# Performance work log

Measured on AMD Instinct MI355X. Metric: run time of the kernel, lower is better.

## Reference

```python
import jax, jax.numpy as jnp
import numpy as np

B, N, D, H, DH, F, L, LC = 32, 256, 512, 8, 64, 2048, 8, 2
NEG = -1e9
SCALE = 1.0 / float(np.sqrt(DH))


def _ln(x, g, b, eps=1e-3):
    # keras LayerNormalization default epsilon=1e-3
    m = jnp.mean(x, -1, keepdims=True)
    v = jnp.mean((x - m) ** 2, -1, keepdims=True)
    return (x - m) * jax.lax.rsqrt(v + eps) * g + b


def setup_inputs() -> dict:
    key = jax.random.key(0)
    ks = jax.random.split(key, 20)
    n = lambda k, s: jax.random.normal(k, s, dtype=jnp.float32) * 0.02
    lengths = jax.random.randint(ks[0], (B,), N // 2, N + 1)
    mask = jnp.arange(N)[None, :] < lengths[:, None]  # [B,N] bool
    return {
        'x': jax.random.normal(ks[1], (B, N, D), dtype=jnp.float32),
        'interaction': jax.random.normal(ks[2], (B, N, N, H), dtype=jnp.float32) * 0.1,
        'class_token': n(ks[3], (1, 1, D)),
        'p_ln1_g': jnp.ones((L, D)), 'p_ln1_b': jnp.zeros((L, D)),
        'p_wq': n(ks[4], (L, D, D)), 'p_wk': n(ks[5], (L, D, D)),
        'p_wv': n(ks[6], (L, D, D)), 'p_wo': n(ks[7], (L, D, D)),
        'p_ln2_g': jnp.ones((L, D)), 'p_ln2_b': jnp.zeros((L, D)),
        'p_w1': n(ks[8], (L, D, F)), 'p_b1': jnp.zeros((L, F)),
        'p_w2': n(ks[9], (L, F, D)), 'p_b2': jnp.zeros((L, D)),
        'c_ln1_g': jnp.ones((LC, D)), 'c_ln1_b': jnp.zeros((LC, D)),
        'c_qk': n(ks[10], (LC, D, H, DH)), 'c_qb': jnp.zeros((LC, H, DH)),
        'c_kk': n(ks[11], (LC, D, H, DH)), 'c_kb': jnp.zeros((LC, H, DH)),
        'c_vk': n(ks[12], (LC, D, H, DH)), 'c_vb': jnp.zeros((LC, H, DH)),
        'c_ok': n(ks[13], (LC, H, DH, D)), 'c_ob': jnp.zeros((LC, D)),
        'c_ln2_g': jnp.ones((LC, D)), 'c_ln2_b': jnp.zeros((LC, D)),
        'c_w1': n(ks[14], (LC, D, F)), 'c_b1': jnp.zeros((LC, F)),
        'c_w2': n(ks[15], (LC, F, D)), 'c_b2': jnp.zeros((LC, D)),
        'mask': mask,
    }


def _part_forward(x, interaction, class_token, p_ln1_g, p_ln1_b, p_wq, p_wk, p_wv, p_wo,
                  p_ln2_g, p_ln2_b, p_w1, p_b1, p_w2, p_b2,
                  c_ln1_g, c_ln1_b, c_qk, c_qb, c_kk, c_kb, c_vk, c_vb, c_ok, c_ob,
                  c_ln2_g, c_ln2_b, c_w1, c_b1, c_w2, c_b2, mask):
    # pairwise particle mask [B,1,N,N]; keras Softmax adds (1-mask)*-1e9
    pmask = (mask[:, None, None, :] & mask[:, None, :, None]).astype(x.dtype)
    padd = (1.0 - pmask) * NEG
    inter = jnp.transpose(interaction, (0, 3, 1, 2))  # [B,H,N,N]
    h = x
    for i in range(L):
        # pre-LN interaction self-attention (dropout inactive at inference)
        hn = _ln(h, p_ln1_g[i], p_ln1_b[i])
        q = (hn @ p_wq[i]).reshape(B, N, H, DH)
        k = (hn @ p_wk[i]).reshape(B, N, H, DH)
        v = (hn @ p_wv[i]).reshape(B, N, H, DH)
        s = jnp.einsum('bqhd,bkhd->bhqk', q, k) * SCALE + inter + padd
        a = jax.nn.softmax(s, axis=-1)
        o = jnp.einsum('bhqk,bkhd->bqhd', a, v).reshape(B, N, D) @ p_wo[i]
        h = h + o
        # pre-LN FFN, gelu (exact, tf.nn.gelu default)
        fn = _ln(h, p_ln2_g[i], p_ln2_b[i])
        h = h + (jax.nn.gelu(fn @ p_w1[i] + p_b1[i], approximate=False) @ p_w2[i] + p_b2[i])
    query = jnp.broadcast_to(class_token, (B, 1, D)).astype(x.dtype)
    cmask = jnp.concatenate([jnp.ones((B, 1), bool), mask], axis=1)[:, None, None, :].astype(x.dtype)
    cadd = (1.0 - cmask) * NEG  # [B,1,1,N+1]
    for i in range(LC):
        # class-attention: K/V from LN(concat([token, particles])), Q from RAW token (as in source)
        cat = jnp.concatenate([query, h], axis=1)  # [B,N+1,D]
        cn = _ln(cat, c_ln1_g[i], c_ln1_b[i])
        qh = jnp.einsum('bqd,dhk->bqhk', query, c_qk[i]) + c_qb[i]
        kh = jnp.einsum('bsd,dhk->bshk', cn, c_kk[i]) + c_kb[i]
        vh = jnp.einsum('bsd,dhk->bshk', cn, c_vk[i]) + c_vb[i]
        s = jnp.einsum('bqhk,bshk->bhqs', qh, kh) * SCALE + cadd
        a = jax.nn.softmax(s, axis=-1)
        o = jnp.einsum('bhqs,bshk->bqhk', a, vh)
        o = jnp.einsum('bqhk,hkd->bqd', o, c_ok[i]) + c_ob[i]
        query = query + o
        fn = _ln(query, c_ln2_g[i], c_ln2_b[i])
        query = query + (jax.nn.gelu(fn @ c_w1[i] + c_b1[i], approximate=False) @ c_w2[i] + c_b2[i])
    return query  # [B,1,D]


def reference(x, interaction, class_token, p_ln1_g, p_ln1_b, p_wq, p_wk, p_wv, p_wo,
              p_ln2_g, p_ln2_b, p_w1, p_b1, p_w2, p_b2,
              c_ln1_g, c_ln1_b, c_qk, c_qb, c_kk, c_kb, c_vk, c_vb, c_ok, c_ob,
              c_ln2_g, c_ln2_b, c_w1, c_b1, c_w2, c_b2, mask):
    return _part_forward(x, interaction, class_token, p_ln1_g, p_ln1_b, p_wq, p_wk, p_wv, p_wo,
                         p_ln2_g, p_ln2_b, p_w1, p_b1, p_w2, p_b2,
                         c_ln1_g, c_ln1_b, c_qk, c_qb, c_kk, c_kb, c_vk, c_vb, c_ok, c_ob,
                         c_ln2_g, c_ln2_b, c_w1, c_b1, c_w2, c_b2, mask)
```

## Files before the change

kernel.cpp:

```cpp
#include <hip/hip_runtime.h>
#include <hip/hip_fp16.h>

#define B_ 32
#define N_ 256
#define D_ 512
#define H_ 8
#define DH_ 64
#define F_ 2048
#define L_ 8
#define LC_ 2
#define NEG_ (-1e9f)
#define SCALE_ 0.125f
#define LDSK 72
#define KCH_ 128

typedef unsigned short u16;
typedef unsigned int u32;
typedef long long s64;
typedef __attribute__((ext_vector_type(8))) short bf16x8;
typedef __attribute__((ext_vector_type(8))) unsigned short u16x8;
typedef __attribute__((ext_vector_type(4))) float f32x4;

__device__ __forceinline__ float b2f(u16 u) {
    union { u32 i; float f; } v; v.i = ((u32)u) << 16; return v.f;
}
__device__ __forceinline__ u16 f2b(float f) {
    union { float f; u32 i; } v; v.f = f;
    u32 x = v.i;
    u32 r = (x + 0x7FFFu + ((x >> 16) & 1u)) >> 16;
    return (u16)r;
}
__device__ __forceinline__ float h2f(u16 u) {
    __half_raw hr; hr.x = u;
    return __half2float(__half(hr));
}
__device__ __forceinline__ void gld16(u16* lds, const u16* g) {
    __builtin_amdgcn_global_load_lds(
        (const __attribute__((address_space(1))) u16*)g,
        (__attribute__((address_space(3))) u16*)lds, 16, 0, 0);
}
__device__ __forceinline__ float ldf(const void* p, size_t i, int fl) {
    if (fl == 1) return ((const float*)p)[i];
    if (fl == 0) return b2f(((const u16*)p)[i]);
    return h2f(((const u16*)p)[i]);
}
__device__ __forceinline__ void ld4(const void* p, size_t i, int fl, float o[4]) {
    if (fl == 1) {
        const float4 v = *(const float4*)((const float*)p + i);
        o[0] = v.x; o[1] = v.y; o[2] = v.z; o[3] = v.w;
    } else if (fl == 0) {
        const ushort4 v = *(const ushort4*)((const u16*)p + i);
        o[0] = b2f(v.x); o[1] = b2f(v.y); o[2] = b2f(v.z); o[3] = b2f(v.w);
    } else {
        const ushort4 v = *(const ushort4*)((const u16*)p + i);
        o[0] = h2f(v.x); o[1] = h2f(v.y); o[2] = h2f(v.z); o[3] = h2f(v.w);
    }
}

__global__ void sniff_kernel(const u32* __restrict__ g1, int* __restrict__ flag) {
    if (threadIdx.x == 0 && blockIdx.x == 0) {
        u32 w = g1[0];
        int f = 0;
        if (w == 0x3F800000u) f = 1;
        else if (w == 0x3C003C00u) f = 2;
        flag[0] = f;
    }
}

__global__ void mask_decode_kernel(const unsigned char* __restrict__ raw,
                                   float* __restrict__ mf) {
    int i = blockIdx.x * 256 + threadIdx.x;
    if (i >= B_ * N_) return;
    unsigned char c0 = raw[0], c1 = raw[1], c4 = raw[4];
    bool v;
    if (c1 == 0x3F || c1 == 0x3C) {
        v = ((const u16*)raw)[i] != 0;
    } else if (c0 == 1 && c1 == 1) {
        v = raw[i] != 0;
    } else if (c0 == 1 && c1 == 0) {
        if (c4 == 1) v = ((const int*)raw)[i] != 0;
        else v = ((const long long*)raw)[i] != 0;
    } else {
        v = ((const float*)raw)[i] != 0.0f;
    }
    mf[i] = v ? 1.0f : 0.0f;
}

__global__ void cvt_in_kernel(const void* __restrict__ in, float* __restrict__ out,
                              int n, const int* __restrict__ fl) {
    int i = blockIdx.x * 256 + threadIdx.x;
    if (i < n) out[i] = ldf(in, (size_t)i, fl[0]);
}
__global__ void bcast_token_kernel(const void* __restrict__ ct, float* __restrict__ qry,
                                   const int* __restrict__ fl) {
    int i = blockIdx.x * 256 + threadIdx.x;
    qry[i] = ldf(ct, (size_t)(i & (D_ - 1)), fl[0]);
}
__global__ void out_copy_kernel(const float* __restrict__ in, float* __restrict__ out, int n) {
    int i = blockIdx.x * 256 + threadIdx.x;
    if (i < n) out[i] = in[i];
}
__global__ void concat_bias_kernel(const void* __restrict__ b1, s64 o1,
                                   const void* __restrict__ b2, s64 o2,
                                   float* __restrict__ dst, const int* __restrict__ flp) {
    int i = blockIdx.x * 256 + threadIdx.x;
    if (i < 512) dst[i] = ldf(b1, (size_t)(o1 + i), flp[0]);
    else if (i < 1024) dst[i] = ldf(b2, (size_t)(o2 + i - 512), flp[0]);
}

__global__ __launch_bounds__(256) void inter_t_kernel(const void* __restrict__ inter,
                                                      const float* __restrict__ mf,
                                                      u16* __restrict__ out,
                                                      const int* __restrict__ flp) {
    __shared__ float tile[256][9];
    __shared__ float mks[256];
    int fl = flp[0];
    int bq = blockIdx.x;
    int b = bq >> 8, q = bq & 255;
    int t = threadIdx.x;
    size_t base = (size_t)bq * 2048;
#pragma unroll
    for (int p = 0; p < 8; ++p) {
        int e = p * 256 + t;
        tile[e >> 3][e & 7] = ldf(inter, base + e, fl);
    }
    mks[t] = mf[b * 256 + t];
    __syncthreads();
    float mq = mf[b * 256 + q];
    int h = t >> 5;
    int k0 = (t & 31) * 8;
    u16x8 v8;
#pragma unroll
    for (int ii = 0; ii < 8; ++ii) {
        int k = k0 + ii;
        float v = tile[k][h];
        if (mq * mks[k] < 0.5f) v += NEG_;
        v8[ii] = (short)f2b(v);
    }
    *(u16x8*)(out + (((size_t)(b * 8 + h) * 256 + q) * 256 + k0)) = v8;
}

__global__ __launch_bounds__(256) void transpose_w_kernel(const void* __restrict__ W, s64 weoff,
                                                          int Nst, int Kd,
                                                          u16* __restrict__ wt,
                                                          const int* __restrict__ flp) {
    __shared__ float tile[32][33];
    int fl = flp[0];
    int n0 = blockIdx.x * 32, k0 = blockIdx.y * 32;
    int tr = threadIdx.x >> 5, tc = threadIdx.x & 31;
#pragma unroll
    for (int p = 0; p < 4; ++p) {
        int kk = p * 8 + tr;
        tile[kk][tc] = ldf(W, (size_t)(weoff + (s64)(k0 + kk) * Nst + n0 + tc), fl);
    }
    __syncthreads();
#pragma unroll
    for (int p = 0; p < 4; ++p) {
        int nn = p * 8 + tr;
        wt[(s64)(n0 + nn) * Kd + k0 + tc] = f2b(tile[tc][nn]);
    }
}

__global__ __launch_bounds__(256) void twt6_kernel(const void* __restrict__ wq,
                                                   const void* __restrict__ wk,
                                                   const void* __restrict__ wv,
                                                   const void* __restrict__ wo,
                                                   const void* __restrict__ w1,
                                                   const void* __restrict__ w2,
                                                   s64 off44, s64 offw1, s64 offw2,
                                                   u16* __restrict__ wtqkv,
                                                   u16* __restrict__ wto,
                                                   u16* __restrict__ wt1,
                                                   u16* __restrict__ wt2,
                                                   const int* __restrict__ flp) {
    __shared__ float tile[32][33];
    int fl = flp[0];
    int bid = blockIdx.x;
    const void* W; s64 weoff; int Nst, Kd; u16* dst; int lb;
    if (bid < 256)       { W = wq; weoff = off44; Nst = 512;  Kd = 512;  dst = wtqkv;          lb = bid; }
    else if (bid < 512)  { W = wk; weoff = off44; Nst = 512;  Kd = 512;  dst = wtqkv + 262144; lb = bid - 256; }
    else if (bid < 768)  { W = wv; weoff = off44; Nst = 512;  Kd = 512;  dst = wtqkv + 524288; lb = bid - 512; }
    else if (bid < 1024) { W = wo; weoff = off44; Nst = 512;  Kd = 512;  dst = wto;            lb = bid - 768; }
    else if (bid < 2048) { W = w1; weoff = offw1; Nst = 2048; Kd = 512;  dst = wt1;            lb = bid - 1024; }
    else                 { W = w2; weoff = offw2; Nst = 512;  Kd = 2048; dst = wt2;            lb = bid - 2048; }
    int nx = Nst >> 5;
    int n0 = (lb % nx) << 5, k0 = (lb / nx) << 5;
    int tr = threadIdx.x >> 5, tc = threadIdx.x & 31;
#pragma unroll
    for (int p = 0; p < 4; ++p) {
        int kk = p * 8 + tr;
        tile[kk][tc] = ldf(W, (size_t)(weoff + (s64)(k0 + kk) * Nst + n0 + tc), fl);
    }
    __syncthreads();
#pragma unroll
    for (int p = 0; p < 4; ++p) {
        int nn = p * 8 + tr;
        dst[(s64)(n0 + nn) * Kd + k0 + tc] = f2b(tile[tc][nn]);
    }
}

__global__ __launch_bounds__(256) void ln_kernel(const float* __restrict__ in,
                                                 const void* __restrict__ g,
                                                 const void* __restrict__ bta,
                                                 s64 peoff,
                                                 u16* __restrict__ out,
                                                 const int* __restrict__ flp) {
    __shared__ float ws4[4];
    __shared__ float wsq[4];
    int fl = flp[0];
    size_t row = blockIdx.x;
    int t = threadIdx.x;
    float x0 = in[row * D_ + t];
    float x1 = in[row * D_ + 256 + t];
    float s = x0 + x1;
#pragma unroll
    for (int off = 32; off > 0; off >>= 1) s += __shfl_xor(s, off);
    if ((t & 63) == 0) ws4[t >> 6] = s;
    __syncthreads();
    float mean = (ws4[0] + ws4[1] + ws4[2] + ws4[3]) * (1.0f / D_);
    float d0 = x0 - mean, d1 = x1 - mean;
    float sq = d0 * d0 + d1 * d1;
#pragma unroll
    for (int off = 32; off > 0; off >>= 1) sq += __shfl_xor(sq, off);
    if ((t & 63) == 0) wsq[t >> 6] = sq;
    __syncthreads();
    float var = (wsq[0] + wsq[1] + wsq[2] + wsq[3]) * (1.0f / D_);
    float inv = 1.0f / sqrtf(var + 1e-3f);
    out[row * D_ + t]       = f2b(d0 * inv * ldf(g, peoff + t, fl)       + ldf(bta, peoff + t, fl));
    out[row * D_ + 256 + t] = f2b(d1 * inv * ldf(g, peoff + 256 + t, fl) + ldf(bta, peoff + 256 + t, fl));
}

__global__ __launch_bounds__(256) void ln_cat_kernel(const float* __restrict__ qry,
                                                     const float* __restrict__ h,
                                                     const void* __restrict__ g,
                                                     const void* __restrict__ bta,
                                                     s64 peoff,
                                                     u16* __restrict__ out,
                                                     const int* __restrict__ flp) {
    __shared__ float ws4[4];
    __shared__ float wsq[4];
    int fl = flp[0];
    size_t row = blockIdx.x;
    int b = (int)(row / 257);
    int r = (int)(row % 257);
    const float* src = (r == 0) ? (qry + (size_t)b * D_)
                                : (h + ((size_t)b * N_ + (r - 1)) * D_);
    int t = threadIdx.x;
    float x0 = src[t];
    float x1 = src[256 + t];
    float s = x0 + x1;
#pragma unroll
    for (int off = 32; off > 0; off >>= 1) s += __shfl_xor(s, off);
    if ((t & 63) == 0) ws4[t >> 6] = s;
    __syncthreads();
    float mean = (ws4[0] + ws4[1] + ws4[2] + ws4[3]) * (1.0f / D_);
    float d0 = x0 - mean, d1 = x1 - mean;
    float sq = d0 * d0 + d1 * d1;
#pragma unroll
    for (int off = 32; off > 0; off >>= 1) sq += __shfl_xor(sq, off);
    if ((t & 63) == 0) wsq[t >> 6] = sq;
    __syncthreads();
    float var = (wsq[0] + wsq[1] + wsq[2] + wsq[3]) * (1.0f / D_);
    float inv = 1.0f / sqrtf(var + 1e-3f);
    out[row * D_ + t]       = f2b(d0 * inv * ldf(g, peoff + t, fl)       + ldf(bta, peoff + t, fl));
    out[row * D_ + 256 + t] = f2b(d1 * inv * ldf(g, peoff + 256 + t, fl) + ldf(bta, peoff + 256 + t, fl));
}

__global__ __launch_bounds__(512) void mfma_gemm_t(const u16* __restrict__ A,
                                                   const u16* __restrict__ Wt,
                                                   int wst, int wkoff,
                                                   const void* __restrict__ bias, s64 beoff,
                                                   int bflag,
                                                   const float* __restrict__ res,
                                                   void* __restrict__ C, int cbf,
                                                   int M, int N, int K, int act,
                                                   const int* __restrict__ flp) {
    __shared__ u16 Alds[2 * 128 * 64];
    __shared__ u16 Blds[2 * 128 * 64];
    int tid = threadIdx.x;
    int gx = gridDim.x;
    int nwg = gx * gridDim.y;
    int orig = blockIdx.y * gx + blockIdx.x;
    int xcd = orig & 7;
    int qq = nwg >> 3, rr = nwg & 7;
    int wg = (xcd < rr ? xcd * (qq + 1) : rr * (qq + 1) + (xcd - rr) * qq) + (orig >> 3);
    int bx = wg % gx, by = wg / gx;
    int bm = by << 7, bn = bx << 7;
    int wid = tid >> 6, lane = tid & 63;
    int wm = (wid >> 2) << 6, wn = (wid & 3) << 5;
    int l15 = lane & 15, q = lane >> 4;
    f32x4 acc[4][2];
#pragma unroll
    for (int a = 0; a < 4; ++a)
#pragma unroll
        for (int b = 0; b < 2; ++b) acc[a][b] = (f32x4){0.f, 0.f, 0.f, 0.f};
    int srow = tid >> 3;
    int sseg = tid & 7;
    int xseg = sseg ^ (srow & 7);
    const u16* arow[2];
#pragma unroll
    for (int p = 0; p < 2; ++p) {
        int gr = bm + p * 64 + srow;
        if (gr >= M) gr = M - 1;
        arow[p] = A + (size_t)gr * K + (xseg << 3);
    }
    const u16* brow[2];
#pragma unroll
    for (int p = 0; p < 2; ++p)
        brow[p] = Wt + (size_t)(bn + p * 64 + srow) * wst + wkoff + (xseg << 3);
    int dstoff = srow * 64 + (sseg << 3);
    auto stage = [&](int buf, int k0) {
        u16* Ab = Alds + buf * 8192;
        u16* Bb = Blds + buf * 8192;
#pragma unroll
        for (int p = 0; p < 2; ++p) gld16(&Ab[dstoff + p * 4096], arow[p] + k0);
#pragma unroll
        for (int p = 0; p < 2; ++p) gld16(&Bb[dstoff + p * 4096], brow[p] + k0);
    };
    int nt = K >> 6;
    stage(0, 0);
    if (nt > 1) stage(1, 64);
    for (int t = 0; t < nt; ++t) {
        if (t + 1 < nt) asm volatile("s_waitcnt vmcnt(4)" ::: "memory");
        else            asm volatile("s_waitcnt vmcnt(0)" ::: "memory");
        __builtin_amdgcn_s_barrier();
        asm volatile("" ::: "memory");
        const u16* Ac = Alds + (t & 1) * 8192;
        const u16* Bc = Blds + (t & 1) * 8192;
#pragma unroll
        for (int ks = 0; ks < 2; ++ks) {
            int seg = ((ks * 4 + q) ^ (l15 & 7)) << 3;
            bf16x8 af[4], bfr[2];
#pragma unroll
            for (int mt = 0; mt < 4; ++mt)
                af[mt] = *(const bf16x8*)(&Ac[(wm + mt * 16 + l15) * 64 + seg]);
#pragma unroll
            for (int nt2 = 0; nt2 < 2; ++nt2)
                bfr[nt2] = *(const bf16x8*)(&Bc[(wn + nt2 * 16 + l15) * 64 + seg]);
#pragma unroll
            for (int mt = 0; mt < 4; ++mt)
#pragma unroll
                for (int nt2 = 0; nt2 < 2; ++nt2)
                    acc[mt][nt2] = __builtin_amdgcn_mfma_f32_16x16x32_bf16(
                        af[mt], bfr[nt2], acc[mt][nt2], 0, 0, 0);
        }
        asm volatile("" ::: "memory");
        __builtin_amdgcn_s_barrier();
        if (t + 2 < nt) stage(t & 1, (t + 2) << 6);
    }
    int fl = (bflag >= 0) ? bflag : flp[0];
#pragma unroll
    for (int nt2 = 0; nt2 < 2; ++nt2) {
        int col = bn + wn + nt2 * 16 + l15;
        float bv = bias ? ldf(bias, (size_t)(beoff + col), fl) : 0.f;
#pragma unroll
        for (int mt = 0; mt < 4; ++mt) {
#pragma unroll
            for (int i = 0; i < 4; ++i) {
                int row = bm + wm + mt * 16 + q * 4 + i;
                if (row >= M) continue;
                float c = acc[mt][nt2][i] + bv;
                if (act) c = 0.5f * c * (1.0f + erff(c * 0.70710678118654752f));
                if (res) c += res[(size_t)row * N + col];
                if (cbf) ((u16*)C)[(size_t)row * N + col] = f2b(c);
                else     ((float*)C)[(size_t)row * N + col] = c;
            }
        }
    }
}

__global__ __launch_bounds__(256) void skinny_gemm_kernel(const void* __restrict__ A, int abf,
                                                          const void* __restrict__ W, s64 weoff,
                                                          int wst,
                                                          float* __restrict__ Cp,
                                                          int N, int K,
                                                          const int* __restrict__ flp) {
    __shared__ float As[32 * KCH_];
    int wfl = flp[0];
    int tid = threadIdx.x;
    int bn = blockIdx.x << 6;
    int ks = blockIdx.y;
    int k0 = ks * KCH_;
#pragma unroll
    for (int p = 0; p < (32 * KCH_) / 1024; ++p) {
        int idx = p * 1024 + tid * 4;
        int m = idx >> 7, c = idx & (KCH_ - 1);
        size_t gi = (size_t)m * K + k0 + c;
        if (abf) {
            const ushort4 v = *(const ushort4*)((const u16*)A + gi);
            As[idx]     = b2f(v.x);
            As[idx + 1] = b2f(v.y);
            As[idx + 2] = b2f(v.z);
            As[idx + 3] = b2f(v.w);
        } else {
            *(float4*)&As[idx] = *(const float4*)((const float*)A + gi);
        }
    }
    __syncthreads();
    int tx = tid & 63, ty = tid >> 6;
    int n = bn + tx;
    float acc[8] = {0.f, 0.f, 0.f, 0.f, 0.f, 0.f, 0.f, 0.f};
#pragma unroll 4
    for (int kk = 0; kk < KCH_; kk += 4) {
        float w0 = ldf(W, (size_t)(weoff + (s64)(k0 + kk) * wst + n), wfl);
        float w1 = ldf(W, (size_t)(weoff + (s64)(k0 + kk + 1) * wst + n), wfl);
        float w2 = ldf(W, (size_t)(weoff + (s64)(k0 + kk + 2) * wst + n), wfl);
        float w3 = ldf(W, (size_t)(weoff + (s64)(k0 + kk + 3) * wst + n), wfl);
#pragma unroll
        for (int r = 0; r < 8; ++r) {
            const float4 a = *(const float4*)&As[(ty * 8 + r) * KCH_ + kk];
            acc[r] += a.x * w0 + a.y * w1 + a.z * w2 + a.w * w3;
        }
    }
#pragma unroll
    for (int r = 0; r < 8; ++r)
        Cp[((size_t)ks * 32 + ty * 8 + r) * N + n] = acc[r];
}

__global__ __launch_bounds__(256) void skinny_epi_kernel(const float* __restrict__ Cp,
                                                         int KS, int N,
                                                         const void* __restrict__ bias, s64 beoff,
                                                         const float* __restrict__ res,
                                                         float* __restrict__ C, int act,
                                                         const int* __restrict__ flp) {
    int i = blockIdx.x * 256 + threadIdx.x;
    if (i >= 32 * N) return;
    int n = i % N;
    float s = 0.f;
    for (int ks = 0; ks < KS; ++ks) s += Cp[(size_t)ks * 32 * N + i];
    if (bias) s += ldf(bias, (size_t)(beoff + n), flp[0]);
    if (act) s = 0.5f * s * (1.0f + erff(s * 0.70710678118654752f));
    if (res) s += res[i];
    C[i] = s;
}

__global__ __launch_bounds__(256) void attn_mfma_kernel(const u16* __restrict__ QKV,
                                                        const u16* __restrict__ IT,
                                                        u16* __restrict__ O) {
    __shared__ u16 KV[256 * 72];
    __shared__ u16 Amat[64 * 264];
    int li = blockIdx.y * 4 + blockIdx.x;
    int slot = li >> 3;
    int bh = (li & 7) * 32 + (slot >> 2);
    int q0 = (slot & 3) << 6;
    int b = bh >> 3, hh = bh & 7;
    int tid = threadIdx.x;
    int w = tid >> 6, l = tid & 63, q2 = l >> 4, l15 = l & 15;
    int qrow = q0 + (w << 4) + l15;
    const u16* qptr = QKV + (size_t)(b * N_ + qrow) * 1536 + hh * DH_ + (q2 << 3);
    bf16x8 aq0 = *(const bf16x8*)(qptr);
    bf16x8 aq1 = *(const bf16x8*)(qptr + 32);
    {
        int r = tid >> 3, seg = (tid & 7) << 3;
#pragma unroll
        for (int p = 0; p < 8; ++p) {
            int k = p * 32 + r;
            *(u16x8*)(&KV[k * LDSK + seg]) =
                *(const u16x8*)(QKV + (size_t)(b * N_ + k) * 1536 + 512 + hh * DH_ + seg);
        }
    }
    u16x8 vreg[8];
    {
        const u16* vptr = QKV + (size_t)(b * N_ + (w << 6)) * 1536 + 1024 + hh * DH_ + l;
#pragma unroll
        for (int s = 0; s < 8; ++s)
#pragma unroll
            for (int e = 0; e < 8; ++e)
                vreg[s][e] = vptr[(size_t)(s * 8 + e) * 1536];
    }
    const u16* itp = IT + ((size_t)bh * N_ + q0 + (w << 4) + (q2 << 2)) * N_ + l15;
    u16 itv0[16], itv1[16], itv2[16], itv3[16];
#pragma unroll
    for (int t = 0; t < 16; ++t) {
        itv0[t] = itp[t * 16];
        itv1[t] = itp[(size_t)N_ + t * 16];
        itv2[t] = itp[(size_t)2 * N_ + t * 16];
        itv3[t] = itp[(size_t)3 * N_ + t * 16];
    }
    asm volatile("s_waitcnt lgkmcnt(0)" ::: "memory");
    __builtin_amdgcn_s_barrier();
    __builtin_amdgcn_sched_barrier(0);
    f32x4 acc[16];
#pragma unroll
    for (int t = 0; t < 16; ++t) {
        const u16* kp = &KV[(t * 16 + l15) * LDSK + (q2 << 3)];
        bf16x8 b0 = *(const bf16x8*)(kp);
        bf16x8 b1 = *(const bf16x8*)(kp + 32);
        f32x4 z = (f32x4){0.f, 0.f, 0.f, 0.f};
        z = __builtin_amdgcn_mfma_f32_16x16x32_bf16(aq0, b0, z, 0, 0, 0);
        acc[t] = __builtin_amdgcn_mfma_f32_16x16x32_bf16(aq1, b1, z, 0, 0, 0);
    }
    asm volatile("s_waitcnt lgkmcnt(0)" ::: "memory");
    __builtin_amdgcn_s_barrier();
    __builtin_amdgcn_sched_barrier(0);
#pragma unroll
    for (int s = 0; s < 8; ++s)
        *(u16x8*)(&KV[l * 264 + (w << 6) + s * 8]) = vreg[s];
    float mx[4] = {-3e38f, -3e38f, -3e38f, -3e38f};
#pragma unroll
    for (int t = 0; t < 16; ++t) {
        float s0 = acc[t][0] * SCALE_ + b2f(itv0[t]);
        float s1 = acc[t][1] * SCALE_ + b2f(itv1[t]);
        float s2 = acc[t][2] * SCALE_ + b2f(itv2[t]);
        float s3 = acc[t][3] * SCALE_ + b2f(itv3[t]);
        acc[t][0] = s0; acc[t][1] = s1; acc[t][2] = s2; acc[t][3] = s3;
        mx[0] = fmaxf(mx[0], s0);
        mx[1] = fmaxf(mx[1], s1);
        mx[2] = fmaxf(mx[2], s2);
        mx[3] = fmaxf(mx[3], s3);
    }
#pragma unroll
    for (int i = 0; i < 4; ++i) {
        mx[i] = fmaxf(mx[i], __shfl_xor(mx[i], 1));
        mx[i] = fmaxf(mx[i], __shfl_xor(mx[i], 2));
        mx[i] = fmaxf(mx[i], __shfl_xor(mx[i], 4));
        mx[i] = fmaxf(mx[i], __shfl_xor(mx[i], 8));
    }
    float sum[4] = {0.f, 0.f, 0.f, 0.f};
#pragma unroll
    for (int t = 0; t < 16; ++t)
#pragma unroll
        for (int i = 0; i < 4; ++i) {
            float e = expf(acc[t][i] - mx[i]);
            acc[t][i] = e;
            sum[i] += e;
        }
#pragma unroll
    for (int i = 0; i < 4; ++i) {
        sum[i] += __shfl_xor(sum[i], 1);
        sum[i] += __shfl_xor(sum[i], 2);
        sum[i] += __shfl_xor(sum[i], 4);
        sum[i] += __shfl_xor(sum[i], 8);
        sum[i] = 1.0f / sum[i];
    }
#pragma unroll
    for (int t = 0; t < 16; ++t)
#pragma unroll
        for (int i = 0; i < 4; ++i)
            Amat[((w << 4) + (q2 << 2) + i) * 264 + t * 16 + l15] = f2b(acc[t][i] * sum[i]);
    asm volatile("s_waitcnt lgkmcnt(0)" ::: "memory");
    __builtin_amdgcn_s_barrier();
    __builtin_amdgcn_sched_barrier(0);
    f32x4 pacc[4];
#pragma unroll
    for (int dt = 0; dt < 4; ++dt) pacc[dt] = (f32x4){0.f, 0.f, 0.f, 0.f};
#pragma unroll
    for (int kc = 0; kc < 8; ++kc) {
        bf16x8 af = *(const bf16x8*)(&Amat[((w << 4) + l15) * 264 + kc * 32 + (q2 << 3)]);
#pragma unroll
        for (int dt = 0; dt < 4; ++dt) {
            bf16x8 bf = *(const bf16x8*)(&KV[(dt * 16 + l15) * 264 + kc * 32 + (q2 << 3)]);
            pacc[dt] = __builtin_amdgcn_mfma_f32_16x16x32_bf16(af, bf, pacc[dt], 0, 0, 0);
        }
    }
    u16* ob = O + (size_t)(b * N_ + q0 + (w << 4) + (q2 << 2)) * D_ + hh * DH_ + l15;
#pragma unroll
    for (int dt = 0; dt < 4; ++dt)
#pragma unroll
        for (int i = 0; i < 4; ++i)
            ob[(size_t)i * D_ + dt * 16] = f2b(pacc[dt][i]);
}

__global__ __launch_bounds__(256) void cls_attn_kernel(const float* __restrict__ qh,
                                                       const u16* __restrict__ kvh,
                                                       const float* __restrict__ mf,
                                                       float* __restrict__ O) {
    __shared__ float qs[64];
    __shared__ float am[257];
    __shared__ float wred[4];
    __shared__ float vred[256];
    int b = blockIdx.x >> 3, hh = blockIdx.x & 7;
    int t = threadIdx.x;
    int w = t >> 6, l = t & 63;
    if (t < 64) qs[t] = qh[(size_t)b * D_ + hh * DH_ + t];
    __syncthreads();
    const u16* krow = kvh + (size_t)(b * 257 + t) * 1024 + hh * DH_;
    float s = 0.f;
#pragma unroll
    for (int seg = 0; seg < 8; ++seg) {
        u16x8 kv8 = *(const u16x8*)(krow + seg * 8);
#pragma unroll
        for (int e = 0; e < 8; ++e) s += qs[seg * 8 + e] * b2f(kv8[e]);
    }
    float cm = (t == 0) ? 1.0f : mf[b * N_ + t - 1];
    s = s * SCALE_ + ((cm > 0.5f) ? 0.0f : NEG_);
    float s256 = -1e30f;
    if (t == 0) {
        const u16* krow2 = kvh + (size_t)(b * 257 + 256) * 1024 + hh * DH_;
        float s2 = 0.f;
#pragma unroll
        for (int seg = 0; seg < 8; ++seg) {
            u16x8 kv8 = *(const u16x8*)(krow2 + seg * 8);
#pragma unroll
            for (int e = 0; e < 8; ++e) s2 += qs[seg * 8 + e] * b2f(kv8[e]);
        }
        float cm2 = mf[b * N_ + 255];
        s256 = s2 * SCALE_ + ((cm2 > 0.5f) ? 0.0f : NEG_);
    }
    float mx = (t == 0) ? fmaxf(s, s256) : s;
#pragma unroll
    for (int off = 32; off > 0; off >>= 1) mx = fmaxf(mx, __shfl_xor(mx, off));
    if (l == 0) wred[w] = mx;
    __syncthreads();
    mx = fmaxf(fmaxf(wred[0], wred[1]), fmaxf(wred[2], wred[3]));
    float p = expf(s - mx);
    float p256 = (t == 0) ? expf(s256 - mx) : 0.f;
    float sum = p + p256;
#pragma unroll
    for (int off = 32; off > 0; off >>= 1) sum += __shfl_xor(sum, off);
    __syncthreads();
    if (l == 0) wred[w] = sum;
    __syncthreads();
    float invs = 1.0f / (wred[0] + wred[1] + wred[2] + wred[3]);
    am[t] = p * invs;
    if (t == 0) am[256] = p256 * invs;
    __syncthreads();
    int g = w, d = l;
    const u16* vcol = kvh + (size_t)(b * 257 + g * 64) * 1024 + 512 + hh * DH_ + d;
    float acc = 0.f;
#pragma unroll 8
    for (int j = 0; j < 64; ++j)
        acc += am[g * 64 + j] * b2f(vcol[(size_t)j * 1024]);
    if (g == 3)
        acc += am[256] * b2f(kvh[(size_t)(b * 257 + 256) * 1024 + 512 + hh * DH_ + d]);
    vred[t] = acc;
    __syncthreads();
    if (t < 64)
        O[(size_t)b * D_ + hh * DH_ + t] = vred[t] + vred[64 + t] + vred[128 + t] + vred[192 + t];
}

extern "C" void kernel_launch(void* const* d_in, const int* in_sizes, int n_in,
                              void* d_out, int out_size, void* d_ws, size_t ws_size,
                              hipStream_t stream) {
    const void* x           = d_in[0];
    const void* interaction = d_in[1];
    const void* class_token = d_in[2];
    const void* p_ln1_g = d_in[3];
    const void* p_ln1_b = d_in[4];
    const void* p_wq    = d_in[5];
    const void* p_wk    = d_in[6];
    const void* p_wv    = d_in[7];
    const void* p_wo    = d_in[8];
    const void* p_ln2_g = d_in[9];
    const void* p_ln2_b = d_in[10];
    const void* p_w1    = d_in[11];
    const void* p_b1    = d_in[12];
    const void* p_w2    = d_in[13];
    const void* p_b2    = d_in[14];
    const void* c_ln1_g = d_in[15];
    const void* c_ln1_b = d_in[16];
    const void* c_qk    = d_in[17];
    const void* c_qb    = d_in[18];
    const void* c_kk    = d_in[19];
    const void* c_kb    = d_in[20];
    const void* c_vk    = d_in[21];
    const void* c_vb    = d_in[22];
    const void* c_ok    = d_in[23];
    const void* c_ob    = d_in[24];
    const void* c_ln2_g = d_in[25];
    const void* c_ln2_b = d_in[26];
    const void* c_w1    = d_in[27];
    const void* c_b1    = d_in[28];
    const void* c_w2    = d_in[29];
    const void* c_b2    = d_in[30];
    const unsigned char* maskraw = (const unsigned char*)d_in[31];

    const size_t NT  = (size_t)B_ * N_;
    const size_t NTD = NT * D_;

    char* base = (char*)d_ws;
    int*   flag   = (int*)base;
    float* maskf  = (float*)(base + 64);
    float* h      = (float*)(base + 64 + 32768);
    u16*   hn     = (u16*)(h + NTD);
    u16*   qkv    = hn + (size_t)B_ * 257 * D_;
    float* qry    = (float*)(qkv + (size_t)8192 * 1536);
    float* qh     = qry + 16384;
    float* ocls   = qh + 16384;
    u16*   fnq    = (u16*)(ocls + 16384);
    float* midc   = (float*)(fnq + 16384);
    float* biaskv = midc + 65536;
    u16*   wt     = (u16*)(biaskv + 1024);
    u16*   wtqkv = wt;
    u16*   wto   = wt + 786432;
    u16*   wt1   = wt + 1048576;
    u16*   wt2   = wt + 2097152;
    u16*   inter_t = wt + 3145728;
    u16*   midp  = qkv;
    float* cpart = (float*)(qkv + (size_t)8224 * 1024);

    auto mgemm = [&](const u16* A, const u16* Wt, int wst, int wkoff,
                     const void* bias, s64 beoff, int bflag, const float* res, void* C, int cbf,
                     int M, int N, int K, int act) {
        dim3 grid(N / 128, (M + 127) / 128);
        mfma_gemm_t<<<grid, 512, 0, stream>>>(A, Wt, wst, wkoff, bias, beoff, bflag,
                                              res, C, cbf, M, N, K, act, flag);
    };
    auto skgemm = [&](const void* A, int abf, const void* W, s64 weoff, int wst,
                      const void* bias, s64 beoff, const float* res, float* C,
                      int N, int K, int act) {
        int KS = K / KCH_;
        skinny_gemm_kernel<<<dim3(N / 64, KS), 256, 0, stream>>>(A, abf, W, weoff, wst,
                                                                 cpart, N, K, flag);
        skinny_epi_kernel<<<(32 * N + 255) / 256, 256, 0, stream>>>(cpart, KS, N, bias, beoff,
                                                                    res, C, act, flag);
    };
    auto twt = [&](const void* W, s64 weoff, int Nst, int Kd, u16* dst) {
        dim3 grid(Nst / 32, Kd / 32);
        transpose_w_kernel<<<grid, 256, 0, stream>>>(W, weoff, Nst, Kd, dst, flag);
    };

    sniff_kernel<<<1, 64, 0, stream>>>((const u32*)p_ln1_g, flag);
    mask_decode_kernel<<<32, 256, 0, stream>>>(maskraw, maskf);
    inter_t_kernel<<<8192, 256, 0, stream>>>(interaction, maskf, inter_t, flag);
    cvt_in_kernel<<<(int)(NTD / 256), 256, 0, stream>>>(x, h, (int)NTD, flag);
    bcast_token_kernel<<<64, 256, 0, stream>>>(class_token, qry, flag);

    for (int i = 0; i < L_; ++i) {
        s64 wo = (s64)i * D_ * D_;
        twt6_kernel<<<3072, 256, 0, stream>>>(p_wq, p_wk, p_wv, p_wo, p_w1, p_w2,
                                              wo, (s64)i * D_ * F_, (s64)i * F_ * D_,
                                              wtqkv, wto, wt1, wt2, flag);
        ln_kernel<<<(int)NT, 256, 0, stream>>>(h, p_ln1_g, p_ln1_b, (s64)i * D_, hn, flag);
        mgemm(hn, wtqkv, D_, 0, nullptr, 0, -1, nullptr, qkv, 1, (int)NT, 1536, D_, 0);
        attn_mfma_kernel<<<dim3(4, B_ * H_), 256, 0, stream>>>(qkv, inter_t, hn);
        mgemm(hn, wto, D_, 0, nullptr, 0, -1, h, h, 0, (int)NT, D_, D_, 0);
        ln_kernel<<<(int)NT, 256, 0, stream>>>(h, p_ln2_g, p_ln2_b, (s64)i * D_, hn, flag);
        for (int c = 0; c < 2; ++c) {
            mgemm(hn, wt1 + (s64)c * 1024 * 512, D_, 0,
                  p_b1, (s64)i * F_ + c * 1024, -1, nullptr, midp, 1,
                  (int)NT, 1024, D_, 1);
            mgemm(midp, wt2, F_, c * 1024,
                  (c == 0) ? p_b2 : nullptr, (s64)i * D_, -1, h, h, 0,
                  (int)NT, D_, 1024, 0);
        }
    }

    for (int i = 0; i < LC_; ++i) {
        s64 wo = (s64)i * D_ * D_;
        twt(c_kk, wo, D_, D_, wtqkv);
        twt(c_vk, wo, D_, D_, wtqkv + 262144);
        concat_bias_kernel<<<4, 256, 0, stream>>>(c_kb, (s64)i * D_, c_vb, (s64)i * D_, biaskv, flag);
        ln_cat_kernel<<<B_ * 257, 256, 0, stream>>>(qry, h, c_ln1_g, c_ln1_b, (s64)i * D_, hn, flag);
        skgemm(qry, 0, c_qk, wo, D_, c_qb, (s64)i * D_, nullptr, qh, D_, D_, 0);
        mgemm(hn, wtqkv, D_, 0, biaskv, 0, 1, nullptr, qkv, 1, B_ * 257, 1024, D_, 0);
        cls_attn_kernel<<<B_ * H_, 256, 0, stream>>>(qh, qkv, maskf, ocls);
        skgemm(ocls, 0, c_ok, wo, D_, c_ob, (s64)i * D_, qry, qry, D_, D_, 0);
        ln_kernel<<<B_, 256, 0, stream>>>(qry, c_ln2_g, c_ln2_b, (s64)i * D_, fnq, flag);
        skgemm(fnq, 1, c_w1, (s64)i * D_ * F_, F_, c_b1, (s64)i * F_, nullptr, midc, F_, D_, 1);
        skgemm(midc, 0, c_w2, (s64)i * F_ * D_, D_, c_b2, (s64)i * D_, qry, qry, D_, F_, 0);
    }

    out_copy_kernel<<<(out_size + 255) / 256, 256, 0, stream>>>(qry, (float*)d_out, out_size);
}
```

Baseline: 2.287 ms.

## Use 4-stage K=32 LDS pipeline in GEMM and merge split FFN GEMMs

The MFMA GEMM moves from a double-buffered K=64 tile to a four-buffer ring of K=32 tiles, with loads issued three steps ahead and a single barrier per iteration. The goal is to hide global-load latency and cut synchronisation stalls. The FFN is no longer split into two F halves. It now writes the full 2048-wide intermediate to a new workspace region and runs one GEMM for each projection, removing launches and the extra read-modify-write of the residual. This adds workspace use past inter_t, and more waitcnt bookkeeping for short K loops.

```diff
diff --git a/kernel.cpp b/kernel.cpp
--- a/kernel.cpp
+++ b/kernel.cpp
@@ -275,8 +275,8 @@
                                                    void* __restrict__ C, int cbf,
                                                    int M, int N, int K, int act,
                                                    const int* __restrict__ flp) {
-    __shared__ u16 Alds[2 * 128 * 64];
-    __shared__ u16 Blds[2 * 128 * 64];
+    __shared__ u16 Alds[4 * 128 * 32];
+    __shared__ u16 Blds[4 * 128 * 32];
     int tid = threadIdx.x;
     int gx = gridDim.x;
     int nwg = gx * gridDim.y;
@@ -294,59 +294,46 @@
     for (int a = 0; a < 4; ++a)
 #pragma unroll
         for (int b = 0; b < 2; ++b) acc[a][b] = (f32x4){0.f, 0.f, 0.f, 0.f};
-    int srow = tid >> 3;
-    int sseg = tid & 7;
-    int xseg = sseg ^ (srow & 7);
-    const u16* arow[2];
-#pragma unroll
-    for (int p = 0; p < 2; ++p) {
-        int gr = bm + p * 64 + srow;
-        if (gr >= M) gr = M - 1;
-        arow[p] = A + (size_t)gr * K + (xseg << 3);
-    }
-    const u16* brow[2];
-#pragma unroll
-    for (int p = 0; p < 2; ++p)
-        brow[p] = Wt + (size_t)(bn + p * 64 + srow) * wst + wkoff + (xseg << 3);
-    int dstoff = srow * 64 + (sseg << 3);
+    int srow = tid >> 2;
+    int sseg = tid & 3;
+    int xseg = sseg ^ (srow & 3);
+    int gr = bm + srow; if (gr >= M) gr = M - 1;
+    const u16* arow = A + (size_t)gr * K + (xseg << 3);
+    const u16* brow = Wt + (size_t)(bn + srow) * wst + wkoff + (xseg << 3);
+    int dstoff = srow * 32 + (sseg << 3);
     auto stage = [&](int buf, int k0) {
-        u16* Ab = Alds + buf * 8192;
-        u16* Bb = Blds + buf * 8192;
-#pragma unroll
-        for (int p = 0; p < 2; ++p) gld16(&Ab[dstoff + p * 4096], arow[p] + k0);
-#pragma unroll
-        for (int p = 0; p < 2; ++p) gld16(&Bb[dstoff + p * 4096], brow[p] + k0);
+        gld16(&Alds[buf * 4096 + dstoff], arow + k0);
+        gld16(&Blds[buf * 4096 + dstoff], brow + k0);
     };
-    int nt = K >> 6;
+    int nt = K >> 5;
     stage(0, 0);
-    if (nt > 1) stage(1, 64);
+    stage(1, 32);
+    stage(2, 64);
+    int sg = (q ^ (l15 & 3)) << 3;
     for (int t = 0; t < nt; ++t) {
-        if (t + 1 < nt) asm volatile("s_waitcnt vmcnt(4)" ::: "memory");
-        else            asm volatile("s_waitcnt vmcnt(0)" ::: "memory");
+        int rem = nt - 1 - t;
+        if (rem >= 2)      asm volatile("s_waitcnt vmcnt(4)" ::: "memory");
+        else if (rem == 1) asm volatile("s_waitcnt vmcnt(2)" ::: "memory");
+        else               asm volatile("s_waitcnt vmcnt(0)" ::: "memory");
         __builtin_amdgcn_s_barrier();
-        asm volatile("" ::: "memory");
-        const u16* Ac = Alds + (t & 1) * 8192;
-        const u16* Bc = Blds + (t & 1) * 8192;
-#pragma unroll
-        for (int ks = 0; ks < 2; ++ks) {
-            int seg = ((ks * 4 + q) ^ (l15 & 7)) << 3;
-            bf16x8 af[4], bfr[2];
-#pragma unroll
-            for (int mt = 0; mt < 4; ++mt)
-                af[mt] = *(const bf16x8*)(&Ac[(wm + mt * 16 + l15) * 64 + seg]);
+        __builtin_amdgcn_sched_barrier(0);
+        if (t + 3 < nt) stage((t + 3) & 3, (t + 3) << 5);
+        const u16* Ac = Alds + (t & 3) * 4096;
+        const u16* Bc = Blds + (t & 3) * 4096;
+        bf16x8 af[4], bfr[2];
+#pragma unroll
+        for (int mt = 0; mt < 4; ++mt)
+            af[mt] = *(const bf16x8*)(&Ac[(wm + mt * 16 + l15) * 32 + sg]);
+#pragma unroll
+        for (int nt2 = 0; nt2 < 2; ++nt2)
+            bfr[nt2] = *(const bf16x8*)(&Bc[(wn + nt2 * 16 + l15) * 32 + sg]);
+#pragma unroll
+        for (int mt = 0; mt < 4; ++mt)
 #pragma unroll
             for (int nt2 = 0; nt2 < 2; ++nt2)
-                bfr[nt2] = *(const bf16x8*)(&Bc[(wn + nt2 * 16 + l15) * 64 + seg]);
-#pragma unroll
-            for (int mt = 0; mt < 4; ++mt)
-#pragma unroll
-                for (int nt2 = 0; nt2 < 2; ++nt2)
-                    acc[mt][nt2] = __builtin_amdgcn_mfma_f32_16x16x32_bf16(
-                        af[mt], bfr[nt2], acc[mt][nt2], 0, 0, 0);
-        }
-        asm volatile("" ::: "memory");
-        __builtin_amdgcn_s_barrier();
-        if (t + 2 < nt) stage(t & 1, (t + 2) << 6);
+                acc[mt][nt2] = __builtin_amdgcn_mfma_f32_16x16x32_bf16(
+                    af[mt], bfr[nt2], acc[mt][nt2], 0, 0, 0);
+        __builtin_amdgcn_sched_barrier(0);
     }
     int fl = (bflag >= 0) ? bflag : flp[0];
 #pragma unroll
@@ -686,7 +673,7 @@
     u16*   wt1   = wt + 1048576;
     u16*   wt2   = wt + 2097152;
     u16*   inter_t = wt + 3145728;
-    u16*   midp  = qkv;
+    u16*   midfull = inter_t + (size_t)B_ * H_ * N_ * N_;
     float* cpart = (float*)(qkv + (size_t)8224 * 1024);
 
     auto mgemm = [&](const u16* A, const u16* Wt, int wst, int wkoff,
@@ -726,14 +713,10 @@
         attn_mfma_kernel<<<dim3(4, B_ * H_), 256, 0, stream>>>(qkv, inter_t, hn);
         mgemm(hn, wto, D_, 0, nullptr, 0, -1, h, h, 0, (int)NT, D_, D_, 0);
         ln_kernel<<<(int)NT, 256, 0, stream>>>(h, p_ln2_g, p_ln2_b, (s64)i * D_, hn, flag);
-        for (int c = 0; c < 2; ++c) {
-            mgemm(hn, wt1 + (s64)c * 1024 * 512, D_, 0,
-                  p_b1, (s64)i * F_ + c * 1024, -1, nullptr, midp, 1,
-                  (int)NT, 1024, D_, 1);
-            mgemm(midp, wt2, F_, c * 1024,
-                  (c == 0) ? p_b2 : nullptr, (s64)i * D_, -1, h, h, 0,
-                  (int)NT, D_, 1024, 0);
-        }
+        mgemm(hn, wt1, D_, 0, p_b1, (s64)i * F_, -1, nullptr, midfull, 1,
+              (int)NT, 2048, D_, 1);
+        mgemm(midfull, wt2, F_, 0, p_b2, (s64)i * D_, -1, h, h, 0,
+              (int)NT, D_, F_, 0);
     }
 
     for (int i = 0; i < LC_; ++i) {
```

After: 2.179 ms. -4.7%, faster.
